# Optimization experiments

Hardware: AMD Instinct MI355X
Metric: run time of the kernel (lower is better)

The kernel has to match this reference:

```python
import jax, jax.numpy as jnp
import numpy as np

B, C, H, W = 8, 3, 1024, 1024


def _cubic_weights(t):
    # Catmull-Rom-style weights used by the torch module
    t2 = t * t
    t3 = t2 * t
    cm1 = (-t3 + 2.0 * t2 - t) / 2.0
    c0 = (3.0 * t3 - 5.0 * t2 + 2.0) / 2.0
    c1 = (-3.0 * t3 + 4.0 * t2 + t) / 2.0
    c2 = 1.0 - (cm1 + c0 + c1)
    return (cm1, c0, c1, c2)


def setup_inputs() -> dict:
    key = jax.random.key(0)
    k1, k2, k3 = jax.random.split(key, 3)
    input_image = jax.random.uniform(k1, (B, C, H, W), dtype=jnp.float32)
    delta_x = jax.random.normal(k2, (B, C, H, W), dtype=jnp.float32)
    delta_y = jax.random.normal(k3, (B, C, H, W), dtype=jnp.float32)
    return {"input_image": input_image, "delta_x": delta_x, "delta_y": delta_y}


def reference(input_image, delta_x, delta_y):
    Bb, Cc, Hh, Ww = input_image.shape
    BXC = Bb * Cc
    # base integer grid, broadcast over (B, C)
    Xg = jnp.arange(Ww, dtype=jnp.float32)          # [W]
    Yg = jnp.arange(Hh, dtype=jnp.float32)[:, None]  # [H,1]
    # normalized coords as in the torch module, then back to pixel coords
    new_X = (Xg + delta_x - Ww / 2.0) / (Ww / 2.0 - 1.0)
    new_Y = (Yg + delta_y - Hh / 2.0) / (Hh / 2.0 - 1.0)
    x_map = (new_X + 1.0) * (Ww - 1) / 2.0  # [B,C,H,W]
    y_map = (new_Y + 1.0) * (Hh - 1) / 2.0

    x0f = jnp.floor(x_map)
    y0f = jnp.floor(y_map)
    tx = x_map - x0f
    ty = y_map - y0f
    x0 = x0f.astype(jnp.int32)
    y0 = y0f.astype(jnp.int32)

    wx = [w.reshape(BXC, Hh * Ww) for w in _cubic_weights(tx)]
    wy = [w.reshape(BXC, Hh * Ww) for w in _cubic_weights(ty)]
    xs = [jnp.clip(x0 + o, 0, Ww - 1).reshape(BXC, Hh * Ww) for o in (-1, 0, 1, 2)]
    ys = [jnp.clip(y0 + o, 0, Hh - 1).reshape(BXC, Hh * Ww) for o in (-1, 0, 1, 2)]

    img = input_image.reshape(BXC, Hh * Ww)
    out = jnp.zeros((BXC, Hh * Ww), dtype=jnp.float32)
    for j in range(4):  # fixed 4x4 taps
        row = jnp.zeros((BXC, Hh * Ww), dtype=jnp.float32)
        yoff = ys[j] * Ww
        for i in range(4):
            vals = jnp.take_along_axis(img, yoff + xs[i], axis=1)
            row = row + wx[i] * vals
        out = out + wy[j] * row
    out = jnp.clip(out, 0.0, 1.0)
    return out.reshape(Bb, Cc, Hh, Ww)
```

## Files before the change

### kernel.cpp

```cpp
#include <hip/hip_runtime.h>


#define HD 1024
#define WD 1024
#define TILE 64
#define HALO 8
#define SROWS 80
#define SSTR 83

__device__ __forceinline__ float cubic_gather_global(
    const float* __restrict__ p, int x0, int y0,
    float wxm1, float wx0, float wx1, float wx2,
    float wym1, float wy0, float wy1, float wy2)
{
    int cx0 = min(max(x0 - 1, 0), WD - 1);
    int cx1 = min(max(x0,     0), WD - 1);
    int cx2 = min(max(x0 + 1, 0), WD - 1);
    int cx3 = min(max(x0 + 2, 0), WD - 1);
    int cy0 = min(max(y0 - 1, 0), HD - 1);
    int cy1 = min(max(y0,     0), HD - 1);
    int cy2 = min(max(y0 + 1, 0), HD - 1);
    int cy3 = min(max(y0 + 2, 0), HD - 1);
    const float* r0 = p + (size_t)cy0 * WD;
    const float* r1 = p + (size_t)cy1 * WD;
    const float* r2 = p + (size_t)cy2 * WD;
    const float* r3 = p + (size_t)cy3 * WD;
    float s0 = wxm1 * r0[cx0] + wx0 * r0[cx1] + wx1 * r0[cx2] + wx2 * r0[cx3];
    float s1 = wxm1 * r1[cx0] + wx0 * r1[cx1] + wx1 * r1[cx2] + wx2 * r1[cx3];
    float s2 = wxm1 * r2[cx0] + wx0 * r2[cx1] + wx1 * r2[cx2] + wx2 * r2[cx3];
    float s3 = wxm1 * r3[cx0] + wx0 * r3[cx1] + wx1 * r3[cx2] + wx2 * r3[cx3];
    return wym1 * s0 + wy0 * s1 + wy1 * s2 + wy2 * s3;
}

__global__ __launch_bounds__(256) void bicubic_tile_kernel(
    const float* __restrict__ img,
    const float* __restrict__ dxp,
    const float* __restrict__ dyp,
    float* __restrict__ out)
{
    __shared__ float sm[SROWS * SSTR];

    const int bx = blockIdx.x * TILE;
    const int by = blockIdx.y * TILE;
    const int plane = blockIdx.z;
    const float* __restrict__ p = img + (size_t)plane * (size_t)(HD * WD);

    const int gx0 = bx - HALO;
    const int gy0 = by - HALO;
    const int tid = threadIdx.x;

    if (gx0 >= 0 && gx0 + SROWS <= WD) {
        for (int s = tid; s < SROWS * (SROWS / 4); s += 256) {
            int r = s / (SROWS / 4);
            int q = s - r * (SROWS / 4);
            int gy = min(max(gy0 + r, 0), HD - 1);
            float4 v = *reinterpret_cast<const float4*>(p + (size_t)gy * WD + gx0 + 4 * q);
            int b = r * SSTR + 4 * q;
            sm[b + 0] = v.x; sm[b + 1] = v.y; sm[b + 2] = v.z; sm[b + 3] = v.w;
        }
    } else {
        for (int s = tid; s < SROWS * SROWS; s += 256) {
            int r = s / SROWS;
            int c = s - r * SROWS;
            int gy = min(max(gy0 + r, 0), HD - 1);
            int gx = min(max(gx0 + c, 0), WD - 1);
            sm[r * SSTR + c] = p[(size_t)gy * WD + gx];
        }
    }
    __syncthreads();

    const int col = bx + (tid & 63);
    const int rbase = by + (tid >> 6);
    const int didx0 = (plane << 20) | (rbase << 10) | col;

    float vdx[16], vdy[16];
    #pragma unroll
    for (int it = 0; it < 16; ++it) {
        vdx[it] = dxp[didx0 + it * 4096];
        vdy[it] = dyp[didx0 + it * 4096];
    }

    const float s = 511.5f / 511.0f;
    const float colA = ((float)col - 512.0f) * s + 511.5f;
    const float yA0 = ((float)rbase - 512.0f) * s + 511.5f;
    const float yStep = 4.0f * s;

    #pragma unroll
    for (int it = 0; it < 16; ++it) {
        const int didx = didx0 + it * 4096;
        const float ddx = vdx[it];
        const float ddy = vdy[it];

        float x_map = fmaf(ddx, s, colA);
        float y_map = fmaf(ddy, s, yA0 + (float)it * yStep);

        float x0f = floorf(x_map);
        float y0f = floorf(y_map);
        float tx = x_map - x0f;
        float ty = y_map - y0f;
        int x0 = (int)x0f;
        int y0 = (int)y0f;

        float tx2 = tx * tx, tx3 = tx2 * tx;
        float wxm1 = (-tx3 + 2.0f * tx2 - tx) * 0.5f;
        float wx0  = (3.0f * tx3 - 5.0f * tx2 + 2.0f) * 0.5f;
        float wx1  = (-3.0f * tx3 + 4.0f * tx2 + tx) * 0.5f;
        float wx2  = 1.0f - (wxm1 + wx0 + wx1);

        float ty2 = ty * ty, ty3 = ty2 * ty;
        float wym1 = (-ty3 + 2.0f * ty2 - ty) * 0.5f;
        float wy0  = (3.0f * ty3 - 5.0f * ty2 + 2.0f) * 0.5f;
        float wy1  = (-3.0f * ty3 + 4.0f * ty2 + ty) * 0.5f;
        float wy2  = 1.0f - (wym1 + wy0 + wy1);

        const int lx = x0 - 1 - gx0;
        const int ly = y0 - 1 - gy0;
        const bool inb = (lx >= 0) & (lx <= SROWS - 4) & (ly >= 0) & (ly <= SROWS - 4);

        float acc;
        if (inb) {
            const float* b = &sm[ly * SSTR + lx];
            float s0 = wxm1 * b[0 * SSTR + 0] + wx0 * b[0 * SSTR + 1] + wx1 * b[0 * SSTR + 2] + wx2 * b[0 * SSTR + 3];
            float s1 = wxm1 * b[1 * SSTR + 0] + wx0 * b[1 * SSTR + 1] + wx1 * b[1 * SSTR + 2] + wx2 * b[1 * SSTR + 3];
            float s2 = wxm1 * b[2 * SSTR + 0] + wx0 * b[2 * SSTR + 1] + wx1 * b[2 * SSTR + 2] + wx2 * b[2 * SSTR + 3];
            float s3 = wxm1 * b[3 * SSTR + 0] + wx0 * b[3 * SSTR + 1] + wx1 * b[3 * SSTR + 2] + wx2 * b[3 * SSTR + 3];
            acc = wym1 * s0 + wy0 * s1 + wy1 * s2 + wy2 * s3;
        } else {
            acc = cubic_gather_global(p, x0, y0, wxm1, wx0, wx1, wx2,
                                      wym1, wy0, wy1, wy2);
        }
        out[didx] = fminf(fmaxf(acc, 0.0f), 1.0f);
    }
}

extern "C" void kernel_launch(void* const* d_in, const int* in_sizes, int n_in,
                              void* d_out, int out_size, void* d_ws, size_t ws_size,
                              hipStream_t stream) {
    const float* img = (const float*)d_in[0];
    const float* dxp = (const float*)d_in[1];
    const float* dyp = (const float*)d_in[2];
    float* out = (float*)d_out;

    const int planes = in_sizes[0] / (HD * WD);
    dim3 grid(WD / TILE, HD / TILE, planes);
    bicubic_tile_kernel<<<grid, 256, 0, stream>>>(img, dxp, dyp, out);
}
```

Before: 94.72 us.

## Stage tile as fp16 pairs with shifted copy and use packed half2 FMA

Converts the shared-memory image tile to __half2 pairs and stores two copies, one aligned and one shifted by a single pixel, so any 4-wide horizontal window can be read as two aligned half2 loads. The vertical reduction runs as packed half2 FMAs, with the horizontal weights applied in fp32 afterwards. This halves LDS reads and VALU work per tap. In exchange, the image values and vertical weights drop to fp16 precision, which may exceed output tolerance, and the staging loop does extra conversions plus an extra scalar global load.

```diff
diff --git a/kernel.cpp b/kernel.cpp
--- a/kernel.cpp
+++ b/kernel.cpp
@@ -1,4 +1,5 @@
 #include <hip/hip_runtime.h>
+#include <hip/hip_fp16.h>
 
 
 #define HD 1024
@@ -6,7 +7,9 @@
 #define TILE 64
 #define HALO 8
 #define SROWS 80
-#define SSTR 83
+#define NPAIR 40
+#define PSTR 41
+#define COFF 3296
 
 __device__ __forceinline__ float cubic_gather_global(
     const float* __restrict__ p, int x0, int y0,
@@ -38,7 +41,7 @@
     const float* __restrict__ dyp,
     float* __restrict__ out)
 {
-    __shared__ float sm[SROWS * SSTR];
+    __shared__ __half2 smp[2 * COFF];
 
     const int bx = blockIdx.x * TILE;
     const int by = blockIdx.y * TILE;
@@ -49,22 +52,38 @@
     const int gy0 = by - HALO;
     const int tid = threadIdx.x;
 
-    if (gx0 >= 0 && gx0 + SROWS <= WD) {
-        for (int s = tid; s < SROWS * (SROWS / 4); s += 256) {
-            int r = s / (SROWS / 4);
-            int q = s - r * (SROWS / 4);
+    if (gx0 >= 0 && gx0 + SROWS < WD) {
+        for (int s = tid; s < SROWS * (NPAIR / 2); s += 256) {
+            int r = s / (NPAIR / 2);
+            int q = s - r * (NPAIR / 2);
             int gy = min(max(gy0 + r, 0), HD - 1);
-            float4 v = *reinterpret_cast<const float4*>(p + (size_t)gy * WD + gx0 + 4 * q);
-            int b = r * SSTR + 4 * q;
-            sm[b + 0] = v.x; sm[b + 1] = v.y; sm[b + 2] = v.z; sm[b + 3] = v.w;
+            const float* rowp = p + (size_t)gy * WD + gx0;
+            float4 v = *reinterpret_cast<const float4*>(rowp + 4 * q);
+            float v4 = rowp[4 * q + 4];
+            int b = r * PSTR + 2 * q;
+            __half h0 = __float2half(v.x), h1 = __float2half(v.y);
+            __half h2 = __float2half(v.z), h3 = __float2half(v.w);
+            __half h4 = __float2half(v4);
+            smp[b]            = __halves2half2(h0, h1);
+            smp[b + 1]        = __halves2half2(h2, h3);
+            smp[COFF + b]     = __halves2half2(h1, h2);
+            smp[COFF + b + 1] = __halves2half2(h3, h4);
         }
     } else {
-        for (int s = tid; s < SROWS * SROWS; s += 256) {
-            int r = s / SROWS;
-            int c = s - r * SROWS;
+        for (int s = tid; s < SROWS * NPAIR; s += 256) {
+            int r = s / NPAIR;
+            int j = s - r * NPAIR;
             int gy = min(max(gy0 + r, 0), HD - 1);
-            int gx = min(max(gx0 + c, 0), WD - 1);
-            sm[r * SSTR + c] = p[(size_t)gy * WD + gx];
+            const float* rowp = p + (size_t)gy * WD;
+            int e0 = min(max(gx0 + 2 * j,     0), WD - 1);
+            int e1 = min(max(gx0 + 2 * j + 1, 0), WD - 1);
+            int e2 = min(max(gx0 + 2 * j + 2, 0), WD - 1);
+            __half h0 = __float2half(rowp[e0]);
+            __half h1 = __float2half(rowp[e1]);
+            __half h2 = __float2half(rowp[e2]);
+            int b = r * PSTR + j;
+            smp[b]        = __halves2half2(h0, h1);
+            smp[COFF + b] = __halves2half2(h1, h2);
         }
     }
     __syncthreads();
@@ -119,12 +138,25 @@
 
         float acc;
         if (inb) {
-            const float* b = &sm[ly * SSTR + lx];
-            float s0 = wxm1 * b[0 * SSTR + 0] + wx0 * b[0 * SSTR + 1] + wx1 * b[0 * SSTR + 2] + wx2 * b[0 * SSTR + 3];
-            float s1 = wxm1 * b[1 * SSTR + 0] + wx0 * b[1 * SSTR + 1] + wx1 * b[1 * SSTR + 2] + wx2 * b[1 * SSTR + 3];
-            float s2 = wxm1 * b[2 * SSTR + 0] + wx0 * b[2 * SSTR + 1] + wx1 * b[2 * SSTR + 2] + wx2 * b[2 * SSTR + 3];
-            float s3 = wxm1 * b[3 * SSTR + 0] + wx0 * b[3 * SSTR + 1] + wx1 * b[3 * SSTR + 2] + wx2 * b[3 * SSTR + 3];
-            acc = wym1 * s0 + wy0 * s1 + wy1 * s2 + wy2 * s3;
+            const __half2* bp = smp + ((lx & 1) ? COFF : 0) + ly * PSTR + (lx >> 1);
+            __half2 d00 = bp[0],        d01 = bp[1];
+            __half2 d10 = bp[PSTR],     d11 = bp[PSTR + 1];
+            __half2 d20 = bp[2 * PSTR], d21 = bp[2 * PSTR + 1];
+            __half2 d30 = bp[3 * PSTR], d31 = bp[3 * PSTR + 1];
+            __half2 w0 = __float2half2_rn(wym1);
+            __half2 w1 = __float2half2_rn(wy0);
+            __half2 w2 = __float2half2_rn(wy1);
+            __half2 w3 = __float2half2_rn(wy2);
+            __half2 accA = __hmul2(w0, d00);
+            __half2 accB = __hmul2(w0, d01);
+            accA = __hfma2(w1, d10, accA);
+            accB = __hfma2(w1, d11, accB);
+            accA = __hfma2(w2, d20, accA);
+            accB = __hfma2(w2, d21, accB);
+            accA = __hfma2(w3, d30, accA);
+            accB = __hfma2(w3, d31, accB);
+            acc = wxm1 * __low2float(accA) + wx0 * __high2float(accA)
+                + wx1 * __low2float(accB) + wx2 * __high2float(accB);
         } else {
             acc = cubic_gather_global(p, x0, y0, wxm1, wx0, wx1, wx2,
                                       wym1, wy0, wy1, wy2);
```

Result: slower. 102.1 us (+7.8%).

## Store shared tile as even/odd-shifted float2 pairs for vectorized tap reads

Applied to the files above, without the earlier changes.

Shared memory now holds two copies of the tile as float2 pairs: one aligned at even columns and one shifted by one column. Each row's four horizontal taps can then be read with two 8-byte LDS loads instead of four scalar loads, whatever the parity of lx. The halo shrinks from 8 to 6 rows and columns to offset the doubled footprint. The trade-off is roughly twice the shared-memory fill work and capacity, and a smaller halo sends more large-displacement samples down the slow global-memory fallback path.

```diff
diff --git a/kernel.cpp b/kernel.cpp
--- a/kernel.cpp
+++ b/kernel.cpp
@@ -4,9 +4,11 @@
 #define HD 1024
 #define WD 1024
 #define TILE 64
-#define HALO 8
-#define SROWS 80
-#define SSTR 83
+#define HALO 6
+#define SROWS 76
+#define NPAIR 40
+#define PSTR2 41
+#define COFF2 3116
 
 __device__ __forceinline__ float cubic_gather_global(
     const float* __restrict__ p, int x0, int y0,
@@ -38,7 +40,7 @@
     const float* __restrict__ dyp,
     float* __restrict__ out)
 {
-    __shared__ float sm[SROWS * SSTR];
+    __shared__ float2 sm2[2 * COFF2];
 
     const int bx = blockIdx.x * TILE;
     const int by = blockIdx.y * TILE;
@@ -49,22 +51,33 @@
     const int gy0 = by - HALO;
     const int tid = threadIdx.x;
 
-    if (gx0 >= 0 && gx0 + SROWS <= WD) {
-        for (int s = tid; s < SROWS * (SROWS / 4); s += 256) {
-            int r = s / (SROWS / 4);
-            int q = s - r * (SROWS / 4);
+    if (gx0 >= 0 && gx0 + 80 <= WD - 1) {
+        for (int s = tid; s < SROWS * 20; s += 256) {
+            int r = s / 20;
+            int q = s - r * 20;
             int gy = min(max(gy0 + r, 0), HD - 1);
-            float4 v = *reinterpret_cast<const float4*>(p + (size_t)gy * WD + gx0 + 4 * q);
-            int b = r * SSTR + 4 * q;
-            sm[b + 0] = v.x; sm[b + 1] = v.y; sm[b + 2] = v.z; sm[b + 3] = v.w;
+            const float* rowp = p + (size_t)gy * WD + gx0;
+            float4 v = *reinterpret_cast<const float4*>(rowp + 4 * q);
+            float v4 = rowp[4 * q + 4];
+            int b = r * PSTR2 + 2 * q;
+            sm2[b]             = make_float2(v.x, v.y);
+            sm2[b + 1]         = make_float2(v.z, v.w);
+            sm2[COFF2 + b]     = make_float2(v.y, v.z);
+            sm2[COFF2 + b + 1] = make_float2(v.w, v4);
         }
     } else {
-        for (int s = tid; s < SROWS * SROWS; s += 256) {
-            int r = s / SROWS;
-            int c = s - r * SROWS;
+        for (int s = tid; s < SROWS * NPAIR; s += 256) {
+            int r = s / NPAIR;
+            int j = s - r * NPAIR;
             int gy = min(max(gy0 + r, 0), HD - 1);
-            int gx = min(max(gx0 + c, 0), WD - 1);
-            sm[r * SSTR + c] = p[(size_t)gy * WD + gx];
+            const float* rowp = p + (size_t)gy * WD;
+            int e0 = min(max(gx0 + 2 * j,     0), WD - 1);
+            int e1 = min(max(gx0 + 2 * j + 1, 0), WD - 1);
+            int e2 = min(max(gx0 + 2 * j + 2, 0), WD - 1);
+            float v0 = rowp[e0], v1 = rowp[e1], v2 = rowp[e2];
+            int b = r * PSTR2 + j;
+            sm2[b]         = make_float2(v0, v1);
+            sm2[COFF2 + b] = make_float2(v1, v2);
         }
     }
     __syncthreads();
@@ -80,10 +93,10 @@
         vdy[it] = dyp[didx0 + it * 4096];
     }
 
-    const float s = 511.5f / 511.0f;
-    const float colA = ((float)col - 512.0f) * s + 511.5f;
-    const float yA0 = ((float)rbase - 512.0f) * s + 511.5f;
-    const float yStep = 4.0f * s;
+    const float sc = 511.5f / 511.0f;
+    const float colA = ((float)col - 512.0f) * sc + 511.5f;
+    const float yA0 = ((float)rbase - 512.0f) * sc + 511.5f;
+    const float yStep = 4.0f * sc;
 
     #pragma unroll
     for (int it = 0; it < 16; ++it) {
@@ -91,8 +104,8 @@
         const float ddx = vdx[it];
         const float ddy = vdy[it];
 
-        float x_map = fmaf(ddx, s, colA);
-        float y_map = fmaf(ddy, s, yA0 + (float)it * yStep);
+        float x_map = fmaf(ddx, sc, colA);
+        float y_map = fmaf(ddy, sc, yA0 + (float)it * yStep);
 
         float x0f = floorf(x_map);
         float y0f = floorf(y_map);
@@ -119,11 +132,15 @@
 
         float acc;
         if (inb) {
-            const float* b = &sm[ly * SSTR + lx];
-            float s0 = wxm1 * b[0 * SSTR + 0] + wx0 * b[0 * SSTR + 1] + wx1 * b[0 * SSTR + 2] + wx2 * b[0 * SSTR + 3];
-            float s1 = wxm1 * b[1 * SSTR + 0] + wx0 * b[1 * SSTR + 1] + wx1 * b[1 * SSTR + 2] + wx2 * b[1 * SSTR + 3];
-            float s2 = wxm1 * b[2 * SSTR + 0] + wx0 * b[2 * SSTR + 1] + wx1 * b[2 * SSTR + 2] + wx2 * b[2 * SSTR + 3];
-            float s3 = wxm1 * b[3 * SSTR + 0] + wx0 * b[3 * SSTR + 1] + wx1 * b[3 * SSTR + 2] + wx2 * b[3 * SSTR + 3];
+            const float2* c = sm2 + ((lx & 1) ? COFF2 : 0) + ly * PSTR2 + (lx >> 1);
+            float2 r0a = c[0],         r0b = c[1];
+            float2 r1a = c[PSTR2],     r1b = c[PSTR2 + 1];
+            float2 r2a = c[2 * PSTR2], r2b = c[2 * PSTR2 + 1];
+            float2 r3a = c[3 * PSTR2], r3b = c[3 * PSTR2 + 1];
+            float s0 = wxm1 * r0a.x + wx0 * r0a.y + wx1 * r0b.x + wx2 * r0b.y;
+            float s1 = wxm1 * r1a.x + wx0 * r1a.y + wx1 * r1b.x + wx2 * r1b.y;
+            float s2 = wxm1 * r2a.x + wx0 * r2a.y + wx1 * r2b.x + wx2 * r2b.y;
+            float s3 = wxm1 * r3a.x + wx0 * r3a.y + wx1 * r3b.x + wx2 * r3b.y;
             acc = wym1 * s0 + wy0 * s1 + wy1 * s2 + wy2 * s3;
         } else {
             acc = cubic_gather_global(p, x0, y0, wxm1, wx0, wx1, wx2,
```

After: 128.8 us. +36.0%, slower.
